# Optimization experiments

Measured on AMD Instinct MI355X. Metric: run time of the kernel, lower is better.

Reference implementation:

```python
import jax, jax.numpy as jnp
import numpy as np

M = 24      # number of DeepGravity sub-models
D_IN = 495  # input feature dim
H = 64      # hidden dim
L = 5       # hidden layers per sub-model


def setup_inputs() -> dict:
    key = jax.random.key(0)
    ks = jax.random.split(key, 7)
    s = 1.0 / np.sqrt(D_IN)
    sh = 1.0 / np.sqrt(H)
    return {
        "x": jax.random.normal(ks[0], (65536, D_IN), dtype=jnp.float32),
        "W_in": jax.random.uniform(ks[1], (M, D_IN, H), jnp.float32, -s, s),
        "b_in": jax.random.uniform(ks[2], (M, H), jnp.float32, -s, s),
        "W_h": jax.random.uniform(ks[3], (M, L, H, H), jnp.float32, -sh, sh),
        "b_h": jax.random.uniform(ks[4], (M, L, H), jnp.float32, -sh, sh),
        "W_out": jax.random.uniform(ks[5], (M, H), jnp.float32, -sh, sh),
        "b_out": jax.random.uniform(ks[6], (M,), jnp.float32, -sh, sh),
    }


def reference(x, W_in, b_in, W_h, b_h, W_out, b_out):
    # Batched input projection across all 24 models: [M, N, H]
    h0 = jnp.einsum("nf,mfh->mnh", x, W_in) + b_in[:, None, :]
    h = h0
    # 5 hidden layers (fixed, structurally distinct weights) as batched GEMMs
    for l in range(L):
        h = jax.nn.relu(jnp.einsum("mnh,mhk->mnk", h, W_h[:, l]) + b_h[:, l][:, None, :])
    h = h + h0  # residual
    # output head: Linear(64,1) + tanh, squeezed -> [M, N]
    out = jnp.tanh(jnp.einsum("mnh,mh->mn", h, W_out) + b_out[:, None])
    return out.T  # [N, M]
```

## Files before the change

### kernel.cpp

```cpp
#include <hip/hip_runtime.h>
#include <hip/hip_bf16.h>

typedef __attribute__((ext_vector_type(8))) short short8;
typedef __attribute__((ext_vector_type(4))) float f32x4;
typedef __attribute__((ext_vector_type(4))) unsigned uint4v;

#define NMODEL 24
#define DIN    495
#define KP     512
#define HID    64
#define NLAY   5

__device__ __forceinline__ short bf16r(float f) {
    unsigned u = __float_as_uint(f);
    u += 0x7fffu + ((u >> 16) & 1u);
    return (short)(u >> 16);
}
__device__ __forceinline__ float bf16f(short s) {
    return __uint_as_float(((unsigned)(unsigned short)s) << 16);
}
__device__ __forceinline__ unsigned pkbf16(float lo, float hi) {
    unsigned r;
    asm("v_cvt_pk_bf16_f32 %0, %1, %2" : "=v"(r) : "v"(lo), "v"(hi));
    return r;
}
__device__ __forceinline__ short8 pack2(f32x4 a, f32x4 b) {
    uint4v w;
    w[0] = pkbf16(a[0], a[1]);
    w[1] = pkbf16(a[2], a[3]);
    w[2] = pkbf16(b[0], b[1]);
    w[3] = pkbf16(b[2], b[3]);
    return __builtin_bit_cast(short8, w);
}

struct __attribute__((packed, aligned(4))) f4a { float v[4]; };

__global__ void dg_convert(const float* __restrict__ W_in,
                           const float* __restrict__ W_h,
                           short* __restrict__ wib, short* __restrict__ whb) {
    int idx = blockIdx.x * 256 + threadIdx.x;
    if (idx < NMODEL * 64 * HID * 8) {
        int t    = idx & 7;
        int hout = (idx >> 3) & 63;
        int kb   = (idx >> 9) & 63;
        int m    = idx >> 15;
        int k    = kb * 8 + t;
        float v  = (k < DIN) ? W_in[((size_t)m * DIN + k) * HID + hout] : 0.f;
        wib[idx] = bf16r(v);
    }
    if (idx < NMODEL * NLAY * 8 * HID * 8) {
        int t    = idx & 7;
        int hout = (idx >> 3) & 63;
        int kb   = (idx >> 9) & 7;
        int ml   = idx >> 12;
        int pk   = 16 * (2 * (kb >> 2) + (t >> 2)) + 4 * (kb & 3) + (t & 3);
        float v  = W_h[((size_t)ml * HID + pk) * HID + hout];
        whb[idx] = bf16r(v);
    }
}

__global__ __launch_bounds__(512, 4) void dg_main(
    const float* __restrict__ x,
    const short* __restrict__ wib, const short* __restrict__ whb,
    const float* __restrict__ b_in, const float* __restrict__ b_h,
    const float* __restrict__ W_out, const float* __restrict__ b_out,
    float* __restrict__ out) {

    __shared__ short xs[64 * KP];

    const int tid  = threadIdx.x;
    const int lane = tid & 63;
    const int w    = tid >> 6;
    const int lrow = lane & 15;
    const int g    = lane >> 4;
    const int rowbase = blockIdx.x * 64;
    const int pair = w >> 1;
    const int hf   = w & 1;
    const int rbase = hf * 32;

    for (int i = 0; i < 8; ++i) {
        int r  = i * 8 + w;
        int k0 = lane * 8;
        const float* xr = x + (size_t)(rowbase + r) * DIN + k0;
        uint4v vw;
        if (k0 + 8 <= DIN) {
            f4a a = *(const f4a*)xr;
            f4a b = *(const f4a*)(xr + 4);
            vw[0] = pkbf16(a.v[0], a.v[1]);
            vw[1] = pkbf16(a.v[2], a.v[3]);
            vw[2] = pkbf16(b.v[0], b.v[1]);
            vw[3] = pkbf16(b.v[2], b.v[3]);
        } else {
            float f[8];
#pragma unroll
            for (int j = 0; j < 8; ++j) f[j] = (k0 + j < DIN) ? xr[j] : 0.f;
            vw[0] = pkbf16(f[0], f[1]);
            vw[1] = pkbf16(f[2], f[3]);
            vw[2] = pkbf16(f[4], f[5]);
            vw[3] = pkbf16(f[6], f[7]);
        }
        int byte = (r * (KP * 2) + k0 * 2) ^ ((r & 7) << 4);
        *(short8*)((char*)xs + byte) = __builtin_bit_cast(short8, vw);
    }
    __syncthreads();

#pragma unroll 1
    for (int mi = 0; mi < 6; ++mi) {
        const int m = pair * 6 + mi;

        f32x4 acc[4][2];
#pragma unroll
        for (int a = 0; a < 4; ++a)
#pragma unroll
            for (int b = 0; b < 2; ++b) acc[a][b] = (f32x4)0.0f;

        const short8* wA = (const short8*)wib + (size_t)m * 64 * 64;
#pragma unroll 2
        for (int skt = 0; skt < 16; ++skt) {
            const int kb = skt * 4 + g;
            short8 afr[4], bfr[2];
#pragma unroll
            for (int icf = 0; icf < 4; ++icf)
                afr[icf] = wA[(size_t)kb * 64 + icf * 16 + lrow];
#pragma unroll
            for (int rf = 0; rf < 2; ++rf) {
                int r = rbase + rf * 16 + lrow;
                int byte = (r * (KP * 2) + skt * 64 + g * 16) ^ ((r & 7) << 4);
                bfr[rf] = *(const short8*)((const char*)xs + byte);
            }
#pragma unroll
            for (int icf = 0; icf < 4; ++icf)
#pragma unroll
                for (int rf = 0; rf < 2; ++rf)
                    acc[icf][rf] = __builtin_amdgcn_mfma_f32_16x16x32_bf16(
                        afr[icf], bfr[rf], acc[icf][rf], 0, 0, 0);
        }

        const float* bi = b_in + m * HID;
#pragma unroll
        for (int icf = 0; icf < 4; ++icf) {
            f32x4 bv = *(const f32x4*)(bi + icf * 16 + g * 4);
#pragma unroll
            for (int rf = 0; rf < 2; ++rf) acc[icf][rf] += bv;
        }

        short8 h0b[2][2];
#pragma unroll
        for (int s = 0; s < 2; ++s)
#pragma unroll
            for (int rf = 0; rf < 2; ++rf)
                h0b[s][rf] = pack2(acc[2 * s][rf], acc[2 * s + 1][rf]);

        const short8* wH = (const short8*)whb + (size_t)m * NLAY * 8 * 64;
        short8 hc[2][2];
#pragma unroll
        for (int s = 0; s < 2; ++s)
#pragma unroll
            for (int rf = 0; rf < 2; ++rf) hc[s][rf] = h0b[s][rf];

        f32x4 hacc[4][2];
#pragma unroll 1
        for (int l = 0; l < NLAY; ++l) {
#pragma unroll
            for (int a = 0; a < 4; ++a)
#pragma unroll
                for (int b = 0; b < 2; ++b) hacc[a][b] = (f32x4)0.0f;
#pragma unroll
            for (int s = 0; s < 2; ++s) {
                const int kb = 4 * s + g;
                short8 afr[4];
#pragma unroll
                for (int icf = 0; icf < 4; ++icf)
                    afr[icf] = wH[(size_t)(l * 8 + kb) * 64 + icf * 16 + lrow];
#pragma unroll
                for (int icf = 0; icf < 4; ++icf)
#pragma unroll
                    for (int rf = 0; rf < 2; ++rf)
                        hacc[icf][rf] = __builtin_amdgcn_mfma_f32_16x16x32_bf16(
                            afr[icf], hc[s][rf], hacc[icf][rf], 0, 0, 0);
            }
            const float* bh = b_h + (size_t)(m * NLAY + l) * HID;
#pragma unroll
            for (int icf = 0; icf < 4; ++icf) {
                f32x4 bv = *(const f32x4*)(bh + icf * 16 + g * 4);
#pragma unroll
                for (int rf = 0; rf < 2; ++rf)
#pragma unroll
                    for (int j = 0; j < 4; ++j)
                        hacc[icf][rf][j] = fmaxf(hacc[icf][rf][j] + bv[j], 0.f);
            }
            if (l != NLAY - 1) {
#pragma unroll
                for (int s = 0; s < 2; ++s)
#pragma unroll
                    for (int rf = 0; rf < 2; ++rf)
                        hc[s][rf] = pack2(hacc[2 * s][rf], hacc[2 * s + 1][rf]);
            }
        }

#pragma unroll
        for (int icf = 0; icf < 4; ++icf)
#pragma unroll
            for (int rf = 0; rf < 2; ++rf)
#pragma unroll
                for (int j = 0; j < 4; ++j)
                    hacc[icf][rf][j] += bf16f(h0b[icf >> 1][rf][(icf & 1) * 4 + j]);

        const float* wo = W_out + m * HID;
        const float bo = b_out[m];
#pragma unroll
        for (int rf = 0; rf < 2; ++rf) {
            float s = 0.f;
#pragma unroll
            for (int icf = 0; icf < 4; ++icf) {
                f32x4 wv = *(const f32x4*)(wo + icf * 16 + g * 4);
#pragma unroll
                for (int j = 0; j < 4; ++j)
                    s += hacc[icf][rf][j] * wv[j];
            }
            s += __shfl_xor(s, 16);
            s += __shfl_xor(s, 32);
            s += bo;
            float e = __expf(2.f * s);
            float o = 1.f - 2.f / (e + 1.f);
            if (g == 0)
                out[(size_t)(rowbase + rbase + rf * 16 + lrow) * NMODEL + m] = o;
        }
    }
}

extern "C" void kernel_launch(void* const* d_in, const int* in_sizes, int n_in,
                              void* d_out, int out_size, void* d_ws, size_t ws_size,
                              hipStream_t stream) {
    const float* x     = (const float*)d_in[0];
    const float* W_in  = (const float*)d_in[1];
    const float* b_in  = (const float*)d_in[2];
    const float* W_h   = (const float*)d_in[3];
    const float* b_h   = (const float*)d_in[4];
    const float* W_out = (const float*)d_in[5];
    const float* b_out = (const float*)d_in[6];
    float* out = (float*)d_out;

    short* wib = (short*)d_ws;
    short* whb = wib + NMODEL * 64 * HID * 8;

    const int N = in_sizes[0] / DIN;

    dg_convert<<<3072, 256, 0, stream>>>(W_in, W_h, wib, whb);
    dg_main<<<N / 64, 512, 0, stream>>>(x, wib, whb, b_in, b_h, W_out, b_out, out);
}
```

Before: 227.0 us.

## Process two sub-models per iteration to interleave independent MFMA chains

Each wave now handles two models at once in both the input projection and the hidden layers. The x fragments are loaded from LDS once and shared by both models, and the two independent accumulator chains are interleaved, which helps hide MFMA and global-load latency. The residual h0 is no longer kept; its contribution to the output head is folded into a precomputed dot product with W_out in fp32. This roughly doubles accumulator register use, which under launch_bounds(512,4) risks spills or lower occupancy.

```diff
diff --git a/kernel.cpp b/kernel.cpp
--- a/kernel.cpp
+++ b/kernel.cpp
@@ -105,126 +105,186 @@
     __syncthreads();
 
 #pragma unroll 1
-    for (int mi = 0; mi < 6; ++mi) {
-        const int m = pair * 6 + mi;
-
-        f32x4 acc[4][2];
+    for (int duo = 0; duo < 3; ++duo) {
+        const int m0 = pair * 6 + duo * 2;
+        const int m1 = m0 + 1;
+
+        f32x4 accA[4][2], accB[4][2];
 #pragma unroll
         for (int a = 0; a < 4; ++a)
 #pragma unroll
-            for (int b = 0; b < 2; ++b) acc[a][b] = (f32x4)0.0f;
-
-        const short8* wA = (const short8*)wib + (size_t)m * 64 * 64;
+            for (int b = 0; b < 2; ++b) {
+                accA[a][b] = (f32x4)0.0f;
+                accB[a][b] = (f32x4)0.0f;
+            }
+
+        const short8* wA0 = (const short8*)wib + (size_t)m0 * 64 * 64;
+        const short8* wA1 = (const short8*)wib + (size_t)m1 * 64 * 64;
 #pragma unroll 2
         for (int skt = 0; skt < 16; ++skt) {
             const int kb = skt * 4 + g;
-            short8 afr[4], bfr[2];
-#pragma unroll
-            for (int icf = 0; icf < 4; ++icf)
-                afr[icf] = wA[(size_t)kb * 64 + icf * 16 + lrow];
+            short8 bfr[2];
 #pragma unroll
             for (int rf = 0; rf < 2; ++rf) {
                 int r = rbase + rf * 16 + lrow;
                 int byte = (r * (KP * 2) + skt * 64 + g * 16) ^ ((r & 7) << 4);
                 bfr[rf] = *(const short8*)((const char*)xs + byte);
             }
+            short8 fA[4], fB[4];
 #pragma unroll
             for (int icf = 0; icf < 4; ++icf)
+                fA[icf] = wA0[(size_t)kb * 64 + icf * 16 + lrow];
+#pragma unroll
+            for (int icf = 0; icf < 4; ++icf)
 #pragma unroll
                 for (int rf = 0; rf < 2; ++rf)
-                    acc[icf][rf] = __builtin_amdgcn_mfma_f32_16x16x32_bf16(
-                        afr[icf], bfr[rf], acc[icf][rf], 0, 0, 0);
-        }
-
-        const float* bi = b_in + m * HID;
+                    accA[icf][rf] = __builtin_amdgcn_mfma_f32_16x16x32_bf16(
+                        fA[icf], bfr[rf], accA[icf][rf], 0, 0, 0);
+#pragma unroll
+            for (int icf = 0; icf < 4; ++icf)
+                fB[icf] = wA1[(size_t)kb * 64 + icf * 16 + lrow];
+#pragma unroll
+            for (int icf = 0; icf < 4; ++icf)
+#pragma unroll
+                for (int rf = 0; rf < 2; ++rf)
+                    accB[icf][rf] = __builtin_amdgcn_mfma_f32_16x16x32_bf16(
+                        fB[icf], bfr[rf], accB[icf][rf], 0, 0, 0);
+        }
+
+        const float* bi0 = b_in + m0 * HID;
+        const float* bi1 = b_in + m1 * HID;
 #pragma unroll
         for (int icf = 0; icf < 4; ++icf) {
-            f32x4 bv = *(const f32x4*)(bi + icf * 16 + g * 4);
-#pragma unroll
-            for (int rf = 0; rf < 2; ++rf) acc[icf][rf] += bv;
-        }
-
-        short8 h0b[2][2];
+            f32x4 bv0 = *(const f32x4*)(bi0 + icf * 16 + g * 4);
+            f32x4 bv1 = *(const f32x4*)(bi1 + icf * 16 + g * 4);
+#pragma unroll
+            for (int rf = 0; rf < 2; ++rf) {
+                accA[icf][rf] += bv0;
+                accB[icf][rf] += bv1;
+            }
+        }
+
+        const float* wo0 = W_out + m0 * HID;
+        const float* wo1 = W_out + m1 * HID;
+        float hpA[2] = {0.f, 0.f}, hpB[2] = {0.f, 0.f};
+#pragma unroll
+        for (int icf = 0; icf < 4; ++icf) {
+            f32x4 wv0 = *(const f32x4*)(wo0 + icf * 16 + g * 4);
+            f32x4 wv1 = *(const f32x4*)(wo1 + icf * 16 + g * 4);
+#pragma unroll
+            for (int rf = 0; rf < 2; ++rf)
+#pragma unroll
+                for (int j = 0; j < 4; ++j) {
+                    hpA[rf] += wv0[j] * accA[icf][rf][j];
+                    hpB[rf] += wv1[j] * accB[icf][rf][j];
+                }
+        }
+
+        short8 hcA[2][2], hcB[2][2];
 #pragma unroll
         for (int s = 0; s < 2; ++s)
 #pragma unroll
-            for (int rf = 0; rf < 2; ++rf)
-                h0b[s][rf] = pack2(acc[2 * s][rf], acc[2 * s + 1][rf]);
-
-        const short8* wH = (const short8*)whb + (size_t)m * NLAY * 8 * 64;
-        short8 hc[2][2];
-#pragma unroll
-        for (int s = 0; s < 2; ++s)
-#pragma unroll
-            for (int rf = 0; rf < 2; ++rf) hc[s][rf] = h0b[s][rf];
-
-        f32x4 hacc[4][2];
+            for (int rf = 0; rf < 2; ++rf) {
+                hcA[s][rf] = pack2(accA[2 * s][rf], accA[2 * s + 1][rf]);
+                hcB[s][rf] = pack2(accB[2 * s][rf], accB[2 * s + 1][rf]);
+            }
+
+        const short8* wH0 = (const short8*)whb + (size_t)m0 * NLAY * 8 * 64;
+        const short8* wH1 = (const short8*)whb + (size_t)m1 * NLAY * 8 * 64;
+        f32x4 haA[4][2], haB[4][2];
 #pragma unroll 1
         for (int l = 0; l < NLAY; ++l) {
 #pragma unroll
             for (int a = 0; a < 4; ++a)
 #pragma unroll
-                for (int b = 0; b < 2; ++b) hacc[a][b] = (f32x4)0.0f;
+                for (int b = 0; b < 2; ++b) {
+                    haA[a][b] = (f32x4)0.0f;
+                    haB[a][b] = (f32x4)0.0f;
+                }
 #pragma unroll
             for (int s = 0; s < 2; ++s) {
                 const int kb = 4 * s + g;
-                short8 afr[4];
+                short8 fA[4], fB[4];
 #pragma unroll
                 for (int icf = 0; icf < 4; ++icf)
-                    afr[icf] = wH[(size_t)(l * 8 + kb) * 64 + icf * 16 + lrow];
+                    fA[icf] = wH0[(size_t)(l * 8 + kb) * 64 + icf * 16 + lrow];
 #pragma unroll
                 for (int icf = 0; icf < 4; ++icf)
 #pragma unroll
                     for (int rf = 0; rf < 2; ++rf)
-                        hacc[icf][rf] = __builtin_amdgcn_mfma_f32_16x16x32_bf16(
-                            afr[icf], hc[s][rf], hacc[icf][rf], 0, 0, 0);
-            }
-            const float* bh = b_h + (size_t)(m * NLAY + l) * HID;
+                        haA[icf][rf] = __builtin_amdgcn_mfma_f32_16x16x32_bf16(
+                            fA[icf], hcA[s][rf], haA[icf][rf], 0, 0, 0);
+#pragma unroll
+                for (int icf = 0; icf < 4; ++icf)
+                    fB[icf] = wH1[(size_t)(l * 8 + kb) * 64 + icf * 16 + lrow];
+#pragma unroll
+                for (int icf = 0; icf < 4; ++icf)
+#pragma unroll
+                    for (int rf = 0; rf < 2; ++rf)
+                        haB[icf][rf] = __builtin_amdgcn_mfma_f32_16x16x32_bf16(
+                            fB[icf], hcB[s][rf], haB[icf][rf], 0, 0, 0);
+            }
+            const float* bh0 = b_h + (size_t)(m0 * NLAY + l) * HID;
+            const float* bh1 = b_h + (size_t)(m1 * NLAY + l) * HID;
 #pragma unroll
             for (int icf = 0; icf < 4; ++icf) {
-                f32x4 bv = *(const f32x4*)(bh + icf * 16 + g * 4);
+                f32x4 bv = *(const f32x4*)(bh0 + icf * 16 + g * 4);
 #pragma unroll
                 for (int rf = 0; rf < 2; ++rf)
 #pragma unroll
                     for (int j = 0; j < 4; ++j)
-                        hacc[icf][rf][j] = fmaxf(hacc[icf][rf][j] + bv[j], 0.f);
+                        haA[icf][rf][j] = fmaxf(haA[icf][rf][j] + bv[j], 0.f);
+            }
+#pragma unroll
+            for (int icf = 0; icf < 4; ++icf) {
+                f32x4 bv = *(const f32x4*)(bh1 + icf * 16 + g * 4);
+#pragma unroll
+                for (int rf = 0; rf < 2; ++rf)
+#pragma unroll
+                    for (int j = 0; j < 4; ++j)
+                        haB[icf][rf][j] = fmaxf(haB[icf][rf][j] + bv[j], 0.f);
             }
             if (l != NLAY - 1) {
 #pragma unroll
                 for (int s = 0; s < 2; ++s)
 #pragma unroll
-                    for (int rf = 0; rf < 2; ++rf)
-                        hc[s][rf] = pack2(hacc[2 * s][rf], hacc[2 * s + 1][rf]);
-            }
-        }
-
-#pragma unroll
-        for (int icf = 0; icf < 4; ++icf)
-#pragma unroll
-            for (int rf = 0; rf < 2; ++rf)
-#pragma unroll
-                for (int j = 0; j < 4; ++j)
-                    hacc[icf][rf][j] += bf16f(h0b[icf >> 1][rf][(icf & 1) * 4 + j]);
-
-        const float* wo = W_out + m * HID;
-        const float bo = b_out[m];
+                    for (int rf = 0; rf < 2; ++rf) {
+                        hcA[s][rf] = pack2(haA[2 * s][rf], haA[2 * s + 1][rf]);
+                        hcB[s][rf] = pack2(haB[2 * s][rf], haB[2 * s + 1][rf]);
+                    }
+            }
+        }
+
+        const float bo0 = b_out[m0];
+        const float bo1 = b_out[m1];
 #pragma unroll
         for (int rf = 0; rf < 2; ++rf) {
-            float s = 0.f;
+            float sA = hpA[rf], sB = hpB[rf];
 #pragma unroll
             for (int icf = 0; icf < 4; ++icf) {
-                f32x4 wv = *(const f32x4*)(wo + icf * 16 + g * 4);
-#pragma unroll
-                for (int j = 0; j < 4; ++j)
-                    s += hacc[icf][rf][j] * wv[j];
-            }
-            s += __shfl_xor(s, 16);
-            s += __shfl_xor(s, 32);
-            s += bo;
-            float e = __expf(2.f * s);
-            float o = 1.f - 2.f / (e + 1.f);
-            if (g == 0)
-                out[(size_t)(rowbase + rbase + rf * 16 + lrow) * NMODEL + m] = o;
+                f32x4 wv0 = *(const f32x4*)(wo0 + icf * 16 + g * 4);
+                f32x4 wv1 = *(const f32x4*)(wo1 + icf * 16 + g * 4);
+#pragma unroll
+                for (int j = 0; j < 4; ++j) {
+                    sA += haA[icf][rf][j] * wv0[j];
+                    sB += haB[icf][rf][j] * wv1[j];
+                }
+            }
+            sA += __shfl_xor(sA, 16);
+            sA += __shfl_xor(sA, 32);
+            sB += __shfl_xor(sB, 16);
+            sB += __shfl_xor(sB, 32);
+            sA += bo0;
+            sB += bo1;
+            float eA = __expf(2.f * sA);
+            float eB = __expf(2.f * sB);
+            float oA = 1.f - 2.f / (eA + 1.f);
+            float oB = 1.f - 2.f / (eB + 1.f);
+            if (g == 0) {
+                size_t row = (size_t)(rowbase + rbase + rf * 16 + lrow);
+                out[row * NMODEL + m0] = oA;
+                out[row * NMODEL + m1] = oB;
+            }
         }
     }
 }
```

Measured after the change: 815.1 us. 3.59x slower.
